# Optimization experiments

Hardware: AMD Instinct MI355X
Metric: run time of the kernel (lower is better)

## Reference

```python
import jax, jax.numpy as jnp
import numpy as np

N_JOINTS = 18

_RELATIVE_JOINT_MAP = np.array([[0,3,2,1,3,3,3,3,3,3,3,3,3,3,3,3,3,3],[3,0,2,3,1,1,3,3,3,3,2,3,2,2,2,3,3,3],[2,2,0,1,1,3,3,3,1,2,2,3,3,3,3,3,3,3],[1,3,1,0,2,3,3,3,2,3,3,3,3,3,3,3,3,3],[3,1,1,2,0,2,3,2,2,3,1,3,3,3,3,3,3,3],[3,1,3,3,2,0,3,3,3,3,3,3,1,1,1,3,3,3],[3,3,3,3,3,3,0,3,2,1,3,3,3,3,3,3,3,3],[3,3,3,3,2,3,3,0,2,3,1,1,3,3,3,2,2,2],[3,3,1,2,2,3,2,2,0,1,1,3,3,3,3,3,3,3],[3,3,2,3,3,3,1,3,1,0,2,3,3,3,3,3,3,3],[3,2,2,3,1,3,3,1,1,2,0,2,3,3,3,3,3,3],[3,3,3,3,3,3,3,1,3,3,2,0,3,3,3,1,1,1],[3,2,3,3,3,1,3,3,3,3,3,3,0,1,2,3,3,3],[3,2,3,3,3,1,3,3,3,3,3,3,1,0,2,3,3,3],[3,2,3,3,3,1,3,3,3,3,3,3,2,2,0,3,3,3],[3,3,3,3,3,3,3,2,3,3,3,1,3,3,3,0,1,2],[3,3,3,3,3,3,3,2,3,3,3,1,3,3,3,1,0,2],[3,3,3,3,3,3,3,2,3,3,3,1,3,3,3,2,2,0]], dtype=np.int32)

DIM = 512
HEADS = 8
DEPTH = DIM // HEADS  # 64
BATCH = 4096


def setup_inputs() -> dict:
    key = jax.random.key(0)
    ks = jax.random.split(key, 10)
    std = 0.02
    return {
        "k": jax.random.normal(ks[0], (BATCH, N_JOINTS, DIM), jnp.float32),
        "v": jax.random.normal(ks[1], (BATCH, N_JOINTS, DIM), jnp.float32),
        "q": jax.random.normal(ks[2], (BATCH, N_JOINTS, DIM), jnp.float32),
        "Wq": jax.random.normal(ks[3], (DIM, DIM), jnp.float32) * (DIM ** -0.5),
        "Wk": jax.random.normal(ks[4], (DIM, DIM), jnp.float32) * (DIM ** -0.5),
        "Wv": jax.random.normal(ks[5], (DIM, DIM), jnp.float32) * (DIM ** -0.5),
        "Wo": jax.random.normal(ks[6], (DIM, DIM), jnp.float32) * (DIM ** -0.5),
        "bo": jnp.zeros((DIM,), jnp.float32),
        "rel_k": jax.random.normal(ks[7], (4, DEPTH), jnp.float32) * std,
        "rel_v": jax.random.normal(ks[8], (4, DEPTH), jnp.float32) * std,
        "joint_map": jnp.asarray(_RELATIVE_JOINT_MAP),
    }


def reference(k, v, q, Wq, Wk, Wv, Wo, bo, rel_k, rel_v, joint_map):
    B, n, dim = q.shape
    h, d = HEADS, DEPTH
    scale = d ** -0.5

    def split_heads(x):  # [B, n, h*d] -> [B, h, n, d]
        return x.reshape(B, n, h, d).transpose(0, 2, 1, 3)

    qh = split_heads(q @ Wq)
    kh = split_heads(k @ Wk)
    vh = split_heads(v @ Wv)

    # gather relative position tables: [n, n, d]
    r_pos_k = rel_k[joint_map]
    r_pos_v = rel_v[joint_map]

    # relative bias sums over heads AND depth of K (faithful to original einsum)
    rel_bias = jnp.einsum('bhid,ijd->bij', kh, r_pos_k)  # [B, n, n]
    dots = (jnp.einsum('bhid,bhjd->bhij', qh, kh) + rel_bias[:, None, :, :]) * scale
    att = jax.nn.softmax(dots, axis=-1)  # [B, h, n, n]

    out = jnp.einsum('bhij,bhjd->bhid', att, vh) + jnp.einsum('bhij,ijd->bhid', att, r_pos_v)
    out = out.transpose(0, 2, 1, 3).reshape(B, n, dim)
    out = out @ Wo + bo
    return out, att
```

## Files before the change

### kernel.cpp

```cpp
#include <hip/hip_runtime.h>
#include <stdint.h>

#define BATCH 4096
#define NJ 18
#define DIMM 512
#define HEADS 8
#define DEPTH 64
#define MROWS (BATCH*NJ)
#define ATT_OFF ((size_t)MROWS*DIMM)
#define LDSP 44

typedef float f32x4 __attribute__((ext_vector_type(4)));
typedef _Float16 f16_t;
typedef _Float16 f16x2 __attribute__((ext_vector_type(2)));
typedef _Float16 f16x4 __attribute__((ext_vector_type(4)));
typedef _Float16 f16x8 __attribute__((ext_vector_type(8)));

__global__ __launch_bounds__(256) void convert_w_kernel(
    const float* __restrict__ W0, const float* __restrict__ W1,
    const float* __restrict__ W2, const float* __restrict__ W3,
    f16_t* __restrict__ T0, f16_t* __restrict__ T1,
    f16_t* __restrict__ T2, f16_t* __restrict__ T3)
{
    const float* W = blockIdx.z == 0 ? W0 : blockIdx.z == 1 ? W1 : blockIdx.z == 2 ? W2 : W3;
    f16_t* T       = blockIdx.z == 0 ? T0 : blockIdx.z == 1 ? T1 : blockIdx.z == 2 ? T2 : T3;
    __shared__ float ld[64][65];
    int k0 = blockIdx.y * 64, n0 = blockIdx.x * 64;
    int tid = threadIdx.x;
    #pragma unroll
    for (int it = 0; it < 16; ++it) {
        int idx = tid + it * 256;
        int kk = idx >> 6, nn = idx & 63;
        ld[kk][nn] = W[(size_t)(k0 + kk) * DIMM + n0 + nn];
    }
    __syncthreads();
    #pragma unroll
    for (int it = 0; it < 16; ++it) {
        int idx = tid + it * 256;
        int nn = idx >> 6, kk = idx & 63;
        T[(size_t)(n0 + nn) * DIMM + k0 + kk] = (f16_t)ld[kk][nn];
    }
}

template <int MODE>
__global__ __launch_bounds__(256) void gemm16_kernel(
    const void* __restrict__ A0, const void* __restrict__ A1,
    const void* __restrict__ A2,
    const f16_t* __restrict__ B0, const f16_t* __restrict__ B1,
    const f16_t* __restrict__ B2,
    void* __restrict__ C0, void* __restrict__ C1, void* __restrict__ C2,
    const float* __restrict__ bias)
{
    const void* Aparm = blockIdx.z == 0 ? A0 : blockIdx.z == 1 ? A1 : A2;
    const f16_t* Bt   = blockIdx.z == 0 ? B0 : blockIdx.z == 1 ? B1 : B2;
    void* Cparm       = blockIdx.z == 0 ? C0 : blockIdx.z == 1 ? C1 : C2;

    const int p = blockIdx.x + (DIMM / 128) * blockIdx.y;
    const int logical = (p & 7) * ((DIMM / 128) * (MROWS / 128) / 8) + (p >> 3);
    const int bn = (logical & 3) * 128;
    const int bm = (logical >> 2) * 128;

    __shared__ __align__(16) f16_t As[128 * LDSP];
    __shared__ __align__(16) f16_t Bs[128 * LDSP];
    const int tid = threadIdx.x;
    const int lane = tid & 63;
    const int wv = tid >> 6;
    const int wm = wv >> 1, wn = wv & 1;
    const int l15 = lane & 15, lg = lane >> 4;

    f32x4 acc[4][4] = {};

    for (int ks = 0; ks < DIMM / 32; ++ks) {
        const int k0 = ks * 32;
        __syncthreads();
        #pragma unroll
        for (int r = 0; r < 2; ++r) {
            int c = tid + r * 256;
            int row = c >> 2, kc = c & 3;
            f16x8 val;
            if constexpr (MODE == 0) {
                const float* A = (const float*)Aparm;
                const f32x4* p4 = (const f32x4*)(A + (size_t)(bm + row) * DIMM + k0 + kc * 8);
                f32x4 a0 = p4[0], a1 = p4[1];
                val[0] = (f16_t)a0[0]; val[1] = (f16_t)a0[1];
                val[2] = (f16_t)a0[2]; val[3] = (f16_t)a0[3];
                val[4] = (f16_t)a1[0]; val[5] = (f16_t)a1[1];
                val[6] = (f16_t)a1[2]; val[7] = (f16_t)a1[3];
            } else {
                const f16_t* A = (const f16_t*)Aparm;
                val = *(const f16x8*)(A + (size_t)(bm + row) * DIMM + k0 + kc * 8);
            }
            *(f16x8*)(&As[row * LDSP + kc * 8]) = val;
            f16x8 bv = *(const f16x8*)(Bt + (size_t)(bn + row) * DIMM + k0 + kc * 8);
            *(f16x8*)(&Bs[row * LDSP + kc * 8]) = bv;
        }
        __syncthreads();
        f16x8 af[4], bfr[4];
        #pragma unroll
        for (int mi = 0; mi < 4; ++mi)
            af[mi] = *(const f16x8*)(&As[(wm * 64 + mi * 16 + l15) * LDSP + lg * 8]);
        #pragma unroll
        for (int ni = 0; ni < 4; ++ni)
            bfr[ni] = *(const f16x8*)(&Bs[(wn * 64 + ni * 16 + l15) * LDSP + lg * 8]);
        #pragma unroll
        for (int mi = 0; mi < 4; ++mi)
            #pragma unroll
            for (int ni = 0; ni < 4; ++ni)
                acc[mi][ni] = __builtin_amdgcn_mfma_f32_16x16x32_f16(
                    af[mi], bfr[ni], acc[mi][ni], 0, 0, 0);
    }

    #pragma unroll
    for (int mi = 0; mi < 4; ++mi) {
        #pragma unroll
        for (int ni = 0; ni < 4; ++ni) {
            int col = bn + wn * 64 + ni * 16 + l15;
            int rowb = bm + wm * 64 + mi * 16 + lg * 4;
            f32x4 v = acc[mi][ni];
            if constexpr (MODE == 1) {
                float* C = (float*)Cparm;
                float bv = bias[col];
                #pragma unroll
                for (int r = 0; r < 4; ++r)
                    C[(size_t)(rowb + r) * DIMM + col] = v[r] + bv;
            } else {
                f16_t* C = (f16_t*)Cparm;
                #pragma unroll
                for (int r = 0; r < 4; ++r)
                    C[(size_t)(rowb + r) * DIMM + col] = (f16_t)v[r];
            }
        }
    }
}

__global__ __launch_bounds__(256, 3) void attn_kernel(
    const f16_t* __restrict__ qh, const f16_t* __restrict__ kh,
    const f16_t* __restrict__ vh,
    const float* __restrict__ rel_k, const float* __restrict__ rel_v,
    const int* __restrict__ jmap,
    float* __restrict__ att_out, f16_t* __restrict__ ao)
{
    const int b = blockIdx.x;
    const int tid = threadIdx.x;
    __shared__ __align__(16) f16_t k_s[NJ * DIMM];
    __shared__ __align__(16) f16_t v_s[NJ * DIMM];
    __shared__ float relk_s[4 * DEPTH];
    __shared__ float relv_s[4 * DEPTH];
    __shared__ int map_s[NJ * NJ];
    __shared__ float ksum_s[NJ * DEPTH];
    __shared__ float t4_s[NJ * 4];

    const size_t base = (size_t)b * (NJ * DIMM);
    const uint4* kg = (const uint4*)(kh + base);
    const uint4* vg = (const uint4*)(vh + base);
    uint4* ks4 = (uint4*)k_s;
    uint4* vs4 = (uint4*)v_s;
    for (int c = tid; c < 2 * NJ * 64; c += 256) {
        int t = c / (NJ * 64);
        int e = c - t * (NJ * 64);
        int m = e & 63;
        int pos = (e & ~63) + (m & 56) + (((m & 7) + (m >> 3)) & 7);
        uint4 val = (t == 0 ? kg : vg)[e];
        (t == 0 ? ks4 : vs4)[pos] = val;
    }
    relk_s[tid & 255] = rel_k[tid & 255];
    relv_s[tid & 255] = rel_v[tid & 255];
    for (int e = tid; e < NJ * NJ; e += 256) map_s[e] = jmap[e];

    const int h = tid / NJ, i = tid - (tid / NJ) * NJ;
    const bool act = tid < HEADS * NJ;
    f16x8 qr[8];
    if (act) {
        const f16x8* qp = (const f16x8*)(qh + base + i * DIMM + h * DEPTH);
        #pragma unroll
        for (int t = 0; t < 8; ++t) qr[t] = qp[t];
    }
    __syncthreads();

    const f16x8* ks8 = (const f16x8*)k_s;
    const f16x8* vs8 = (const f16x8*)v_s;

    for (int e = tid; e < NJ * DEPTH; e += 256) {
        int ii = e >> 6, dd = e & 63;
        int tt = dd >> 3, d7 = dd & 7;
        float s = 0.f;
        #pragma unroll
        for (int hh = 0; hh < HEADS; ++hh)
            s += (float)k_s[((ii << 6) + (hh << 3) + ((tt + hh) & 7)) * 8 + d7];
        ksum_s[e] = s;
    }
    __syncthreads();
    if (tid < NJ * 4) {
        int ii = tid >> 2, c = tid & 3;
        float s = 0.f;
        #pragma unroll
        for (int dd = 0; dd < DEPTH; ++dd)
            s += ksum_s[ii * DEPTH + dd] * relk_s[c * DEPTH + dd];
        t4_s[tid] = s;
    }
    __syncthreads();

    if (!act) return;

    float att[NJ];
    float m = -1e30f;
    #pragma unroll
    for (int j = 0; j < NJ; ++j) {
        float s = 0.f;
        #pragma unroll
        for (int t = 0; t < 8; ++t) {
            f16x8 kv = ks8[(j << 6) + (h << 3) + ((t + h) & 7)];
            f16x8 a = qr[t];
            #pragma unroll
            for (int e = 0; e < 8; ++e) s += (float)a[e] * (float)kv[e];
        }
        s += t4_s[i * 4 + map_s[i * NJ + j]];
        s *= 0.125f;
        att[j] = s;
        m = fmaxf(m, s);
    }
    float sum = 0.f;
    #pragma unroll
    for (int j = 0; j < NJ; ++j) { att[j] = __expf(att[j] - m); sum += att[j]; }
    const float inv = 1.f / sum;
    float s4[4] = {0.f, 0.f, 0.f, 0.f};
    float* ap = att_out + (((size_t)b * HEADS + h) * NJ + i) * NJ;
    #pragma unroll
    for (int j = 0; j < NJ; ++j) {
        float a = att[j] * inv;
        att[j] = a;
        ap[j] = a;
        int c = map_s[i * NJ + j];
        s4[0] += (c == 0) ? a : 0.f;
        s4[1] += (c == 1) ? a : 0.f;
        s4[2] += (c == 2) ? a : 0.f;
        s4[3] += (c == 3) ? a : 0.f;
    }

    f16x8* aop = (f16x8*)(ao + base + i * DIMM + h * DEPTH);
    #pragma unroll
    for (int half = 0; half < 2; ++half) {
        float acc[32] = {};
        #pragma unroll
        for (int j = 0; j < NJ; ++j) {
            float a = att[j];
            #pragma unroll
            for (int t = 0; t < 4; ++t) {
                int tt = half * 4 + t;
                f16x8 vv = vs8[(j << 6) + (h << 3) + ((tt + h) & 7)];
                #pragma unroll
                for (int e = 0; e < 8; ++e) acc[t * 8 + e] += a * (float)vv[e];
            }
        }
        #pragma unroll
        for (int c = 0; c < 4; ++c) {
            float sc = s4[c];
            #pragma unroll
            for (int d = 0; d < 32; ++d)
                acc[d] += sc * relv_s[c * DEPTH + half * 32 + d];
        }
        #pragma unroll
        for (int t = 0; t < 4; ++t) {
            f16x8 res;
            #pragma unroll
            for (int e = 0; e < 8; ++e) res[e] = (f16_t)acc[t * 8 + e];
            aop[half * 4 + t] = res;
        }
    }
}

extern "C" void kernel_launch(void* const* d_in, const int* in_sizes, int n_in,
                              void* d_out, int out_size, void* d_ws, size_t ws_size,
                              hipStream_t stream) {
    (void)in_sizes; (void)n_in; (void)out_size; (void)ws_size;
    const float* k_in = (const float*)d_in[0];
    const float* v_in = (const float*)d_in[1];
    const float* q_in = (const float*)d_in[2];
    const float* Wq   = (const float*)d_in[3];
    const float* Wk   = (const float*)d_in[4];
    const float* Wv   = (const float*)d_in[5];
    const float* Wo   = (const float*)d_in[6];
    const float* bo   = (const float*)d_in[7];
    const float* relk = (const float*)d_in[8];
    const float* relv = (const float*)d_in[9];
    const int*   jmap = (const int*)d_in[10];

    char* ws = (char*)d_ws;
    const size_t WT = (size_t)DIMM * DIMM * sizeof(f16_t);
    f16_t* Tq = (f16_t*)(ws + 0 * WT);
    f16_t* Tk = (f16_t*)(ws + 1 * WT);
    f16_t* Tv = (f16_t*)(ws + 2 * WT);
    f16_t* To = (f16_t*)(ws + 3 * WT);
    const size_t PSZ = (size_t)MROWS * DIMM * sizeof(f16_t);
    f16_t* qh = (f16_t*)(ws + 4 * WT + 0 * PSZ);
    f16_t* kh = (f16_t*)(ws + 4 * WT + 1 * PSZ);
    f16_t* vh = (f16_t*)(ws + 4 * WT + 2 * PSZ);
    f16_t* ao = vh;

    float* outp = (float*)d_out;
    float* attp = outp + ATT_OFF;

    convert_w_kernel<<<dim3(8, 8, 4), 256, 0, stream>>>(
        Wq, Wk, Wv, Wo, Tq, Tk, Tv, To);

    gemm16_kernel<0><<<dim3(DIMM / 128, MROWS / 128, 3), 256, 0, stream>>>(
        q_in, k_in, v_in, Tq, Tk, Tv, qh, kh, vh, nullptr);

    attn_kernel<<<BATCH, 256, 0, stream>>>(qh, kh, vh, relk, relv, jmap, attp, ao);

    gemm16_kernel<1><<<dim3(DIMM / 128, MROWS / 128, 1), 256, 0, stream>>>(
        ao, nullptr, nullptr, To, nullptr, nullptr, outp, nullptr, nullptr, bo);
}
```

Before: 485.9 us.

## Pre-tile and XOR-swizzle fp16 operands, load GEMM tiles directly to LDS

Weights are converted into a blocked 128x64 tile layout with an XOR swizzle. The attention kernel writes its output in the same tiled, swizzled layout to a separate workspace buffer instead of reusing vh. The GEMM now uses a K-step of 64 and loads the B tiles (and the A tiles in the fp16 mode) with global_load_lds straight into LDS, reading them back at swizzled offsets to avoid bank conflicts. This is meant to cut register staging and the number of LDS store instructions. In exchange it needs extra workspace and uses larger shared tiles.

```diff
diff --git a/kernel.cpp b/kernel.cpp
--- a/kernel.cpp
+++ b/kernel.cpp
@@ -8,13 +8,14 @@
 #define DEPTH 64
 #define MROWS (BATCH*NJ)
 #define ATT_OFF ((size_t)MROWS*DIMM)
-#define LDSP 44
 
 typedef float f32x4 __attribute__((ext_vector_type(4)));
 typedef _Float16 f16_t;
-typedef _Float16 f16x2 __attribute__((ext_vector_type(2)));
-typedef _Float16 f16x4 __attribute__((ext_vector_type(4)));
 typedef _Float16 f16x8 __attribute__((ext_vector_type(8)));
+
+__device__ __forceinline__ void gl_lds16(const unsigned int* g, unsigned int* l) {
+    __builtin_amdgcn_global_load_lds(g, l, 16, 0, 0);
+}
 
 __global__ __launch_bounds__(256) void convert_w_kernel(
     const float* __restrict__ W0, const float* __restrict__ W1,
@@ -34,11 +35,18 @@
         ld[kk][nn] = W[(size_t)(k0 + kk) * DIMM + n0 + nn];
     }
     __syncthreads();
-    #pragma unroll
-    for (int it = 0; it < 16; ++it) {
-        int idx = tid + it * 256;
-        int nn = idx >> 6, kk = idx & 63;
-        T[(size_t)(n0 + nn) * DIMM + k0 + kk] = (f16_t)ld[kk][nn];
+    f16x8* T8 = (f16x8*)T;
+    #pragma unroll
+    for (int it = 0; it < 2; ++it) {
+        int c = tid + it * 256;
+        int nn = c >> 3, c8 = c & 7;
+        int n = n0 + nn, k = k0 + c8 * 8;
+        f16x8 val;
+        #pragma unroll
+        for (int e = 0; e < 8; ++e) val[e] = (f16_t)ld[c8 * 8 + e][nn];
+        size_t vi = (size_t)((n >> 7) * 8 + (k >> 6)) * 1024
+                  + (n & 127) * 8 + (((k >> 3) & 7) ^ (n & 7));
+        T8[vi] = val;
     }
 }
 
@@ -55,59 +63,87 @@
     const f16_t* Bt   = blockIdx.z == 0 ? B0 : blockIdx.z == 1 ? B1 : B2;
     void* Cparm       = blockIdx.z == 0 ? C0 : blockIdx.z == 1 ? C1 : C2;
 
-    const int p = blockIdx.x + (DIMM / 128) * blockIdx.y;
-    const int logical = (p & 7) * ((DIMM / 128) * (MROWS / 128) / 8) + (p >> 3);
+    const int p = blockIdx.x + 4 * blockIdx.y;
+    const int logical = (p & 7) * (2304 / 8) + (p >> 3);
     const int bn = (logical & 3) * 128;
     const int bm = (logical >> 2) * 128;
 
-    __shared__ __align__(16) f16_t As[128 * LDSP];
-    __shared__ __align__(16) f16_t Bs[128 * LDSP];
+    __shared__ __align__(16) f16_t As[MODE == 0 ? 128 * 72 : 128 * 64];
+    __shared__ __align__(16) f16_t Bs[128 * 64];
+
     const int tid = threadIdx.x;
     const int lane = tid & 63;
     const int wv = tid >> 6;
     const int wm = wv >> 1, wn = wv & 1;
     const int l15 = lane & 15, lg = lane >> 4;
+    const int swz = (l15 & 7) << 4;
+    const int koffb[2] = { (lg * 16) ^ swz, (lg * 16 + 64) ^ swz };
 
     f32x4 acc[4][4] = {};
 
-    for (int ks = 0; ks < DIMM / 32; ++ks) {
-        const int k0 = ks * 32;
+    for (int ks = 0; ks < 8; ++ks) {
         __syncthreads();
-        #pragma unroll
-        for (int r = 0; r < 2; ++r) {
-            int c = tid + r * 256;
-            int row = c >> 2, kc = c & 3;
-            f16x8 val;
-            if constexpr (MODE == 0) {
-                const float* A = (const float*)Aparm;
-                const f32x4* p4 = (const f32x4*)(A + (size_t)(bm + row) * DIMM + k0 + kc * 8);
+        {
+            const unsigned int* btile =
+                (const unsigned int*)(Bt + (size_t)((bn >> 7) * 8 + ks) * 8192);
+            unsigned int* bs = (unsigned int*)Bs;
+            #pragma unroll
+            for (int it = 0; it < 4; ++it) {
+                int chunk = wv * 4 + it;
+                gl_lds16(btile + chunk * 256 + lane * 4, bs + chunk * 256);
+            }
+        }
+        if constexpr (MODE == 0) {
+            const float* A = (const float*)Aparm;
+            #pragma unroll
+            for (int r = 0; r < 4; ++r) {
+                int c = tid + r * 256;
+                int row = c >> 3, kc = c & 7;
+                const f32x4* p4 = (const f32x4*)(A + (size_t)(bm + row) * DIMM + ks * 64 + kc * 8);
                 f32x4 a0 = p4[0], a1 = p4[1];
+                f16x8 val;
                 val[0] = (f16_t)a0[0]; val[1] = (f16_t)a0[1];
                 val[2] = (f16_t)a0[2]; val[3] = (f16_t)a0[3];
                 val[4] = (f16_t)a1[0]; val[5] = (f16_t)a1[1];
                 val[6] = (f16_t)a1[2]; val[7] = (f16_t)a1[3];
-            } else {
-                const f16_t* A = (const f16_t*)Aparm;
-                val = *(const f16x8*)(A + (size_t)(bm + row) * DIMM + k0 + kc * 8);
-            }
-            *(f16x8*)(&As[row * LDSP + kc * 8]) = val;
-            f16x8 bv = *(const f16x8*)(Bt + (size_t)(bn + row) * DIMM + k0 + kc * 8);
-            *(f16x8*)(&Bs[row * LDSP + kc * 8]) = bv;
+                *(f16x8*)(&As[row * 72 + kc * 8]) = val;
+            }
+        } else {
+            const unsigned int* atile =
+                (const unsigned int*)((const f16_t*)Aparm + (size_t)((bm >> 7) * 8 + ks) * 8192);
+            unsigned int* as = (unsigned int*)As;
+            #pragma unroll
+            for (int it = 0; it < 4; ++it) {
+                int chunk = wv * 4 + it;
+                gl_lds16(atile + chunk * 256 + lane * 4, as + chunk * 256);
+            }
         }
         __syncthreads();
-        f16x8 af[4], bfr[4];
-        #pragma unroll
-        for (int mi = 0; mi < 4; ++mi)
-            af[mi] = *(const f16x8*)(&As[(wm * 64 + mi * 16 + l15) * LDSP + lg * 8]);
-        #pragma unroll
-        for (int ni = 0; ni < 4; ++ni)
-            bfr[ni] = *(const f16x8*)(&Bs[(wn * 64 + ni * 16 + l15) * LDSP + lg * 8]);
-        #pragma unroll
-        for (int mi = 0; mi < 4; ++mi)
-            #pragma unroll
-            for (int ni = 0; ni < 4; ++ni)
-                acc[mi][ni] = __builtin_amdgcn_mfma_f32_16x16x32_f16(
-                    af[mi], bfr[ni], acc[mi][ni], 0, 0, 0);
+
+        #pragma unroll
+        for (int kk = 0; kk < 2; ++kk) {
+            const int koff = koffb[kk];
+            f16x8 af[4], bfr[4];
+            #pragma unroll
+            for (int mi = 0; mi < 4; ++mi) {
+                int row = wm * 64 + mi * 16 + l15;
+                if constexpr (MODE == 0)
+                    af[mi] = *(const f16x8*)(&As[row * 72 + kk * 32 + lg * 8]);
+                else
+                    af[mi] = *(const f16x8*)((const char*)As + row * 128 + koff);
+            }
+            #pragma unroll
+            for (int ni = 0; ni < 4; ++ni) {
+                int row = wn * 64 + ni * 16 + l15;
+                bfr[ni] = *(const f16x8*)((const char*)Bs + row * 128 + koff);
+            }
+            #pragma unroll
+            for (int mi = 0; mi < 4; ++mi)
+                #pragma unroll
+                for (int ni = 0; ni < 4; ++ni)
+                    acc[mi][ni] = __builtin_amdgcn_mfma_f32_16x16x32_f16(
+                        af[mi], bfr[ni], acc[mi][ni], 0, 0, 0);
+        }
     }
 
     #pragma unroll
@@ -237,7 +273,9 @@
         s4[3] += (c == 3) ? a : 0.f;
     }
 
-    f16x8* aop = (f16x8*)(ao + base + i * DIMM + h * DEPTH);
+    const size_t grow = (size_t)b * NJ + i;
+    f16x8* aot = (f16x8*)ao + ((grow >> 7) * 8 + h) * 1024 + (grow & 127) * 8;
+    const int rr7 = (int)(grow & 7);
     #pragma unroll
     for (int half = 0; half < 2; ++half) {
         float acc[32] = {};
@@ -264,7 +302,7 @@
             f16x8 res;
             #pragma unroll
             for (int e = 0; e < 8; ++e) res[e] = (f16_t)acc[t * 8 + e];
-            aop[half * 4 + t] = res;
+            aot[(half * 4 + t) ^ rr7] = res;
         }
     }
 }
@@ -295,7 +333,7 @@
     f16_t* qh = (f16_t*)(ws + 4 * WT + 0 * PSZ);
     f16_t* kh = (f16_t*)(ws + 4 * WT + 1 * PSZ);
     f16_t* vh = (f16_t*)(ws + 4 * WT + 2 * PSZ);
-    f16_t* ao = vh;
+    f16_t* ao = (f16_t*)(ws + 4 * WT + 3 * PSZ);
 
     float* outp = (float*)d_out;
     float* attp = outp + ATT_OFF;
```

New measurement: 447.8 us. 7.8% less time.
